# Performance work log

Measured on AMD Instinct MI355X. Metric: run time of the kernel, lower is better.

Reference implementation:

```python
import jax, jax.numpy as jnp
import numpy as np

EPS = 1e-6


def setup_inputs() -> dict:
    key = jax.random.key(0)
    ks = jax.random.split(key, 5)
    B, NH, S, DQK, DV = 2, 8, 1024, 256, 512
    return {
        "q": jax.random.normal(ks[0], (B, NH, S, DQK), dtype=jnp.float32),
        "k": jax.random.normal(ks[1], (B, NH, S, DQK), dtype=jnp.float32),
        "v": jax.random.normal(ks[2], (B, NH, S, DV), dtype=jnp.float32),
        "i_preact": jax.random.normal(ks[3], (B, NH, S), dtype=jnp.float32),
        "f_preact": jax.random.normal(ks[4], (B, NH, S), dtype=jnp.float32),
    }


def reference(q, k, v, i_preact, f_preact):
    B, NH, S, DQK = q.shape
    DV = v.shape[-1]
    inv_sqrt_d = jnp.asarray(1.0 / np.sqrt(DQK), dtype=q.dtype)
    eps = jnp.asarray(EPS, dtype=q.dtype)

    C0 = jnp.zeros((B, NH, DQK, DV), dtype=q.dtype)
    n0 = jnp.zeros((B, NH, DQK), dtype=q.dtype)
    m0 = jnp.zeros((B, NH), dtype=q.dtype)

    def step(carry, xs):
        C, n, m = carry
        q_t, k_t, v_t, i_t, f_t = xs  # [B,NH,DQK],[B,NH,DQK],[B,NH,DV],[B,NH],[B,NH]
        # f_log = -log(1 + exp(-f)) = log_sigmoid(f)
        f_log = jax.nn.log_sigmoid(f_t)
        m_new = jnp.maximum(f_log + m, i_t)
        f_gate = jnp.exp(f_log + m - m_new)
        i_gate = jnp.exp(i_t - m_new)
        kv_outer = k_t[..., :, None] * v_t[..., None, :]  # [B,NH,DQK,DV]
        C = f_gate[..., None, None] * C + i_gate[..., None, None] * kv_outer
        n = f_gate[..., None] * n + i_gate[..., None] * k_t
        q_scaled = q_t * inv_sqrt_d
        h_num = jnp.einsum("bhdv,bhd->bhv", C, q_scaled)
        qn_dot = jnp.sum(n * q_scaled, axis=-1, keepdims=True)  # [B,NH,1]
        h_den = jnp.maximum(jnp.abs(qn_dot), jnp.exp(-m_new)[..., None]) + eps
        h_t = h_num / h_den
        return (C, n, m_new), h_t

    # time-major scan over S
    xs = (
        jnp.moveaxis(q, 2, 0),
        jnp.moveaxis(k, 2, 0),
        jnp.moveaxis(v, 2, 0),
        jnp.moveaxis(i_preact, 2, 0),
        jnp.moveaxis(f_preact, 2, 0),
    )
    (C, n, m), h_tm = jax.lax.scan(step, (C0, n0, m0), xs)
    h = jnp.moveaxis(h_tm, 0, 2)  # [B,NH,S,DV]
    return h, C, n, m
```

## Files before the change

kernel.cpp:

```cpp
#include <hip/hip_runtime.h>
#include <math.h>

#define SEQ   1024
#define DQ    256
#define DVD   512
#define NHH   16
#define EPSF  1e-6f
#define INV_SQRT_D 0.0625f

typedef __attribute__((ext_vector_type(8)))  short short8v;
typedef __attribute__((ext_vector_type(16))) float f32x16;

#define WS_FG    0
#define WS_IG    (NHH*SEQ)
#define WS_ELIM  (2*NHH*SEQ)
#define WS_HDEN  (3*NHH*SEQ)
#define WS_AT    (4*NHH*SEQ)
#define WS_CS    (5*NHH*SEQ)
#define WS_UT    (6*NHH*SEQ)
#define WS_AC    (7*NHH*SEQ)
#define WS_BVEC  (WS_AC + NHH*16)
#define WS_SMALL_FLOATS (WS_BVEC + NHH*16*DQ)

#define QBF_OFF  ((size_t)WS_SMALL_FLOATS * 4)
#define KBF_OFF  (QBF_OFF + (size_t)NHH*SEQ*DQ*2)
#define VTB_OFF  (KBF_OFF + (size_t)NHH*SEQ*DQ*2)
#define KUT_OFF  (VTB_OFF + (size_t)NHH*DVD*SEQ*2)

__device__ __forceinline__ unsigned short f2bf(float f) {
  unsigned int u = __float_as_uint(f);
  return (unsigned short)((u + 0x7fffu + ((u >> 16) & 1u)) >> 16);
}

__device__ __forceinline__ void gl_lds16(const void* g, void* l) {
  __builtin_amdgcn_global_load_lds(
      (const __attribute__((address_space(1))) unsigned int*)g,
      (__attribute__((address_space(3))) unsigned int*)l, 16, 0, 0);
}

__global__ __launch_bounds__(1024) void gates_kernel(
    const float* __restrict__ ipre, const float* __restrict__ fpre,
    float* __restrict__ ws, float* __restrict__ m_out) {
  const int hh = blockIdx.x;
  const int t  = threadIdx.x;
  const int lane = t & 63, wid = t >> 6;
  __shared__ float Fs[SEQ];
  __shared__ float Ms[SEQ];
  __shared__ float wsum[16];
  __shared__ float wmax[16];

  const float fp = fpre[hh*SEQ + t];
  const float ip = ipre[hh*SEQ + t];
  const float flog = fminf(fp, 0.f) - log1pf(expf(-fabsf(fp)));

  float v = flog;
  #pragma unroll
  for (int off = 1; off < 64; off <<= 1) {
    float o = __shfl_up(v, off, 64);
    if (lane >= off) v += o;
  }
  if (lane == 63) wsum[wid] = v;
  __syncthreads();
  float woff = 0.f;
  #pragma unroll
  for (int i = 0; i < 16; ++i) { float s = wsum[i]; if (i < wid) woff += s; }
  const float F = v + woff;
  Fs[t] = F;

  float zm = ip - F;
  #pragma unroll
  for (int off = 1; off < 64; off <<= 1) {
    float o = __shfl_up(zm, off, 64);
    if (lane >= off) zm = fmaxf(zm, o);
  }
  if (lane == 63) wmax[wid] = zm;
  __syncthreads();
  float zoff = -INFINITY;
  #pragma unroll
  for (int i = 0; i < 16; ++i) { float s = wmax[i]; if (i < wid) zoff = fmaxf(zoff, s); }
  const float zfull = fmaxf(zm, zoff);
  const float m_t = F + fmaxf(zfull, 0.f);
  Ms[t] = m_t;
  __syncthreads();

  const float m_prev = (t == 0) ? 0.f : Ms[t - 1];
  const float F_end = Fs[SEQ-1], m_end = Ms[SEQ-1];

  ws[WS_FG   + hh*SEQ + t] = expf(flog + m_prev - m_t);
  ws[WS_IG   + hh*SEQ + t] = expf(ip - m_t);
  ws[WS_ELIM + hh*SEQ + t] = expf(-m_t);
  ws[WS_AT   + hh*SEQ + t] = F - m_t;
  ws[WS_CS   + hh*SEQ + t] = ip - F;
  ws[WS_UT   + hh*SEQ + t] = expf(F_end - F + ip - m_end);
  if (t == SEQ - 1) m_out[hh] = m_t;
  if ((t & 63) == 63) {
    const int c = t >> 6;
    const float Fprev  = (c == 0) ? 0.f : Fs[t - 64];
    const float mprevc = (c == 0) ? 0.f : Ms[t - 64];
    ws[WS_AC + hh*16 + c] = expf((F - Fprev) + (mprevc - m_t));
  }
}

__global__ __launch_bounds__(256) void prep_kernel(
    const float* __restrict__ kin, const float* __restrict__ vin,
    float* __restrict__ ws,
    unsigned short* __restrict__ k_bf, unsigned short* __restrict__ vt_bf,
    unsigned short* __restrict__ kut) {
  __shared__ float lk[64][257];
  const int b = blockIdx.x;
  if (b < 256) {
    const int hh = b >> 4, c = b & 15;
    const int d = threadIdx.x;
    const int tbase = hh*SEQ + c*64;
    const size_t base = (size_t)tbase * DQ;
    #pragma unroll 4
    for (int tt = 0; tt < 64; ++tt) {
      const float val = kin[base + (size_t)tt*DQ + d];
      lk[tt][d] = val;
      k_bf[base + (size_t)tt*DQ + d] = f2bf(val);
    }
    __syncthreads();
    const float* fg = ws + WS_FG + tbase;
    const float* ig = ws + WS_IG + tbase;
    float nb = 0.f;
    #pragma unroll 8
    for (int tt = 0; tt < 64; ++tt) nb = fg[tt]*nb + ig[tt]*lk[tt][d];
    ws[WS_BVEC + (hh*16 + c)*DQ + d] = nb;
    const float* u = ws + WS_UT + tbase;
    #pragma unroll
    for (int g = 0; g < 8; ++g) {
      short8v pk;
      #pragma unroll
      for (int j = 0; j < 8; ++j) {
        const int tt = g*8 + j;
        pk[j] = (short)f2bf(u[tt] * lk[tt][d]);
      }
      *(short8v*)(kut + ((size_t)(hh*DQ + d))*SEQ + c*64 + g*8) = pk;
    }
  } else {
    const int b2 = b - 256;
    const int hh = b2 >> 5, tg = b2 & 31;
    const int tx = threadIdx.x & 31, ty = threadIdx.x >> 5;
    float (*tile)[33] = (float(*)[33])lk;
    for (int vt = 0; vt < 16; ++vt) {
      #pragma unroll
      for (int i = 0; i < 4; ++i)
        tile[ty + 8*i][tx] =
            vin[((size_t)(hh*SEQ + tg*32 + ty + 8*i))*DVD + vt*32 + tx];
      __syncthreads();
      #pragma unroll
      for (int i = 0; i < 4; ++i)
        vt_bf[((size_t)(hh*DVD + vt*32 + ty + 8*i))*SEQ + tg*32 + tx] =
            f2bf(tile[tx][ty + 8*i]);
      __syncthreads();
    }
  }
}

__global__ __launch_bounds__(256) void hden_kernel(
    const float* __restrict__ kin, const float* __restrict__ qin,
    float* __restrict__ ws, unsigned short* __restrict__ q_bf,
    float* __restrict__ n_out) {
  const int hh = blockIdx.x >> 4;
  const int c  = blockIdx.x & 15;
  const int d  = threadIdx.x;
  __shared__ float pbuf[64][DQ];
  __shared__ float spart[64][4];

  float n = 0.f;
  for (int j = 0; j < c; ++j)
    n = ws[WS_AC + hh*16 + j]*n + ws[WS_BVEC + (hh*16 + j)*DQ + d];
  if (c == 15) {
    const float nf = ws[WS_AC + hh*16 + 15]*n +
                     ws[WS_BVEC + (hh*16 + 15)*DQ + d];
    n_out[hh*DQ + d] = nf;
  }

  const int tbase = hh*SEQ + c*64;
  const size_t base = (size_t)tbase * DQ;
  #pragma unroll 4
  for (int tt = 0; tt < 64; ++tt) {
    const float fg = ws[WS_FG + tbase + tt];
    const float ig = ws[WS_IG + tbase + tt];
    n = fg*n + ig*kin[base + (size_t)tt*DQ + d];
    const float qv = qin[base + (size_t)tt*DQ + d];
    q_bf[base + (size_t)tt*DQ + d] = f2bf(qv * INV_SQRT_D);
    pbuf[tt][d] = n * qv;
  }
  __syncthreads();

  {
    const int tt = d >> 2, qd = d & 3;
    float s = 0.f;
    #pragma unroll 8
    for (int j = 0; j < 64; ++j)
      s += pbuf[tt][qd*64 + ((j + d) & 63)];
    spart[tt][qd] = s;
  }
  __syncthreads();
  if (d < 64) {
    const float tot = (spart[d][0] + spart[d][1]) + (spart[d][2] + spart[d][3]);
    const float qn = tot * INV_SQRT_D;
    const float hd = fmaxf(fabsf(qn), ws[WS_ELIM + tbase + d]) + EPSF;
    ws[WS_HDEN + tbase + d] = hd;
  }
}

__global__ __launch_bounds__(512, 2) void attn_kernel(
    const unsigned short* __restrict__ q_bf,
    const unsigned short* __restrict__ k_bf,
    const unsigned short* __restrict__ vt_bf,
    const float* __restrict__ ws,
    float* __restrict__ h_out) {
  const int b = blockIdx.x;
  const int phase = b >> 8;
  const int idx = b & 255;
  const int hh = idx & 15;
  const int vh = (idx >> 4) & 1;
  const int qq = idx >> 5;
  const int qi = phase ? (15 - qq) : qq;
  const int nch = (qi >> 1) + 1;

  const int tid = threadIdx.x;
  const int w = tid >> 6, lane = tid & 63, l31 = lane & 31, hl = lane >> 5;
  const int tsub = w >> 2;
  const int sblk = w & 3;
  const int vsub = w & 3;

  __shared__ unsigned short Klds[128*256];
  __shared__ unsigned short Vtlds[256*128];
  __shared__ unsigned short Plds[64*128];
  __shared__ float c_lds[128];

  const float* a_g  = ws + WS_AT;
  const float* c_g  = ws + WS_CS;
  const float* hd_g = ws + WS_HDEN;

  const int tq = qi*64 + tsub*32 + l31;
  const float a_t = a_g[hh*SEQ + tq];

  short8v qfrag[16];
  #pragma unroll
  for (int d = 0; d < 16; ++d)
    qfrag[d] = *(const short8v*)(q_bf + ((size_t)(hh*SEQ + tq))*DQ + d*16 + hl*8);

  f32x16 acc0 = {}, acc1 = {};

  auto stage = [&](int c) {
    const int s0 = c*128;
    #pragma unroll
    for (int p = 0; p < 8; ++p) {
      int u = p*512 + tid;
      int row = u >> 5, slot = u & 31;
      const unsigned short* src = k_bf +
          ((size_t)(hh*SEQ + s0 + row))*DQ + ((slot ^ (row & 31))*8);
      gl_lds16(src, (char*)Klds + (p*8 + w)*1024);
    }
    #pragma unroll
    for (int p = 0; p < 8; ++p) {
      int u = p*512 + tid;
      int row = u >> 4, slot = u & 15;
      const unsigned short* src = vt_bf +
          ((size_t)(hh*DVD + vh*256 + row))*SEQ + s0 + ((slot ^ (row & 15))*8);
      gl_lds16(src, (char*)Vtlds + (p*8 + w)*1024);
    }
    if (tid < 128) c_lds[tid] = c_g[hh*SEQ + s0 + tid];
  };

  stage(0);
  __syncthreads();

  for (int c = 0; c < nch; ++c) {
    const int s0 = c*128;
    f32x16 sacc = {};
    const int srow = sblk*32 + l31;
    #pragma unroll
    for (int d = 0; d < 16; ++d) {
      short8v af = *(const short8v*)&Klds[srow*256 + (((d*2 + hl) ^ (srow & 31))*8)];
      sacc = __builtin_amdgcn_mfma_f32_32x32x16_bf16(af, qfrag[d], sacc, 0, 0, 0);
    }
    const int prow = tsub*32 + l31;
    #pragma unroll
    for (int i = 0; i < 8; ++i) {
      const int r0 = 2*i;
      const int sl = sblk*32 + (r0 & 3) + 8*(r0 >> 2) + 4*hl;
      const int sg = s0 + sl;
      const float c0 = c_lds[sl];
      const float c1 = c_lds[sl + 1];
      const float p0 = (sg     <= tq) ? __expf(a_t + c0) * sacc[r0]     : 0.f;
      const float p1 = (sg + 1 <= tq) ? __expf(a_t + c1) * sacc[r0 + 1] : 0.f;
      unsigned int pk;
      asm volatile("v_cvt_pk_bf16_f32 %0, %1, %2" : "=v"(pk) : "v"(p0), "v"(p1));
      const int byte = sl*2;
      const int slot = byte >> 4, rem = byte & 15;
      *(unsigned int*)((char*)Plds + prow*256 + ((slot ^ (prow & 15))<<4) + rem) = pk;
    }
    __syncthreads();

    #pragma unroll
    for (int ss = 0; ss < 8; ++ss) {
      const int arow = tsub*32 + l31;
      short8v pa = *(const short8v*)&Plds[arow*128 + (((ss*2 + hl) ^ (arow & 15))*8)];
      const int vr0 = vsub*64 + l31;
      const int slotB = (ss*2 + hl) ^ (l31 & 15);
      short8v vb0 = *(const short8v*)&Vtlds[vr0*128 + slotB*8];
      short8v vb1 = *(const short8v*)&Vtlds[(vr0 + 32)*128 + slotB*8];
      acc0 = __builtin_amdgcn_mfma_f32_32x32x16_bf16(pa, vb0, acc0, 0, 0, 0);
      acc1 = __builtin_amdgcn_mfma_f32_32x32x16_bf16(pa, vb1, acc1, 0, 0, 0);
    }
    __syncthreads();
    if (c + 1 < nch) { stage(c + 1); __syncthreads(); }
  }

  #pragma unroll
  for (int r = 0; r < 16; ++r) {
    const int tl = tsub*32 + (r & 3) + 8*(r >> 2) + 4*hl;
    const int tg = qi*64 + tl;
    const float inv = 1.0f / hd_g[hh*SEQ + tg];
    const size_t ob = ((size_t)(hh*SEQ + tg))*DVD + vh*256 + vsub*64 + l31;
    h_out[ob]      = acc0[r] * inv;
    h_out[ob + 32] = acc1[r] * inv;
  }
}

__global__ __launch_bounds__(256, 2) void cgemm_kernel(
    const unsigned short* __restrict__ kut,
    const unsigned short* __restrict__ vt,
    float* __restrict__ C_out) {
  const int b = blockIdx.x;
  const int hh = b >> 4;
  const int mt = (b >> 3) & 1;
  const int nt = b & 7;
  const int tid = threadIdx.x;
  const int w = tid >> 6, lane = tid & 63, l31 = lane & 31, hl = lane >> 5;
  const int mr = w >> 1;
  const int nc = w & 1;

  __shared__ unsigned short Alds[128*64];
  __shared__ unsigned short Blds[64*64];

  f32x16 acc0 = {}, acc1 = {};
  for (int c = 0; c < 16; ++c) {
    const int t0 = c*64;
    #pragma unroll
    for (int p = 0; p < 4; ++p) {
      int u = p*256 + tid; int row = u >> 3, slot = u & 7;
      const unsigned short* src = kut +
          ((size_t)(hh*DQ + mt*128 + row))*SEQ + t0 + ((slot ^ (row & 7))*8);
      gl_lds16(src, (char*)Alds + (p*4 + w)*1024);
    }
    #pragma unroll
    for (int p = 0; p < 2; ++p) {
      int u = p*256 + tid; int row = u >> 3, slot = u & 7;
      const unsigned short* src = vt +
          ((size_t)(hh*DVD + nt*64 + row))*SEQ + t0 + ((slot ^ (row & 7))*8);
      gl_lds16(src, (char*)Blds + (p*4 + w)*1024);
    }
    __syncthreads();
    #pragma unroll
    for (int ks = 0; ks < 4; ++ks) {
      const int br = nc*32 + l31;
      short8v bf_ = *(const short8v*)&Blds[br*64 + (((ks*2 + hl) ^ (br & 7))*8)];
      const int ar0 = mr*64 + l31, ar1 = ar0 + 32;
      short8v a0 = *(const short8v*)&Alds[ar0*64 + (((ks*2 + hl) ^ (ar0 & 7))*8)];
      short8v a1 = *(const short8v*)&Alds[ar1*64 + (((ks*2 + hl) ^ (ar1 & 7))*8)];
      acc0 = __builtin_amdgcn_mfma_f32_32x32x16_bf16(a0, bf_, acc0, 0, 0, 0);
      acc1 = __builtin_amdgcn_mfma_f32_32x32x16_bf16(a1, bf_, acc1, 0, 0, 0);
    }
    __syncthreads();
  }
  #pragma unroll
  for (int r = 0; r < 16; ++r) {
    const int dl = (r & 3) + 8*(r >> 2) + 4*hl;
    const int d0 = mt*128 + mr*64 + dl;
    const size_t ob = ((size_t)(hh*DQ + d0))*DVD + nt*64 + nc*32 + l31;
    C_out[ob]            = acc0[r];
    C_out[ob + 32*DVD]   = acc1[r];
  }
}

extern "C" void kernel_launch(void* const* d_in, const int* in_sizes, int n_in,
                              void* d_out, int out_size, void* d_ws, size_t ws_size,
                              hipStream_t stream) {
  const float* q  = (const float*)d_in[0];
  const float* k  = (const float*)d_in[1];
  const float* v  = (const float*)d_in[2];
  const float* ip = (const float*)d_in[3];
  const float* fp = (const float*)d_in[4];

  float* h_out = (float*)d_out;
  float* C_out = h_out + (size_t)NHH*SEQ*DVD;
  float* n_out = C_out + (size_t)NHH*DQ*DVD;
  float* m_out = n_out + NHH*DQ;
  float* ws    = (float*)d_ws;

  unsigned short* q_bf  = (unsigned short*)((char*)d_ws + QBF_OFF);
  unsigned short* k_bf  = (unsigned short*)((char*)d_ws + KBF_OFF);
  unsigned short* vt_bf = (unsigned short*)((char*)d_ws + VTB_OFF);
  unsigned short* kut   = (unsigned short*)((char*)d_ws + KUT_OFF);

  gates_kernel<<<NHH, 1024, 0, stream>>>(ip, fp, ws, m_out);
  prep_kernel<<<768, 256, 0, stream>>>(k, v, ws, k_bf, vt_bf, kut);
  hden_kernel<<<NHH*16, 256, 0, stream>>>(k, q, ws, q_bf, n_out);
  attn_kernel<<<512, 512, 0, stream>>>(q_bf, k_bf, vt_bf, ws, h_out);
  cgemm_kernel<<<256, 256, 0, stream>>>(kut, vt_bf, C_out);
}
```

Measured before the change: 100.7 us.

## Fuse gate scan into prep kernel and pair causal query tiles per block

The separate gates kernel is removed. Each k-prep block now recomputes the full per-head log-sigmoid prefix sum and running max over 1024 steps, and keeps its chunk's forget, input and u gates in shared memory instead of reading them from the workspace. Block 0 of each head still writes the shared gate arrays to the workspace. The attention kernel goes from 512 to 256 blocks, and each block handles a long and a short causal query tile (15-pr and pr) in sequence so the work per block is even. This saves one launch and a global round trip but adds redundant scan work per block, and it halves the number of attention blocks resident at once.

Result: no change. 99.73 us (-0.9%).

```diff
diff --git a/kernel.cpp b/kernel.cpp
--- a/kernel.cpp
+++ b/kernel.cpp
@@ -17,8 +17,7 @@
 #define WS_HDEN  (3*NHH*SEQ)
 #define WS_AT    (4*NHH*SEQ)
 #define WS_CS    (5*NHH*SEQ)
-#define WS_UT    (6*NHH*SEQ)
-#define WS_AC    (7*NHH*SEQ)
+#define WS_AC    (6*NHH*SEQ)
 #define WS_BVEC  (WS_AC + NHH*16)
 #define WS_SMALL_FLOATS (WS_BVEC + NHH*16*DQ)
 
@@ -38,102 +37,136 @@
       (__attribute__((address_space(3))) unsigned int*)l, 16, 0, 0);
 }
 
-__global__ __launch_bounds__(1024) void gates_kernel(
-    const float* __restrict__ ipre, const float* __restrict__ fpre,
-    float* __restrict__ ws, float* __restrict__ m_out) {
-  const int hh = blockIdx.x;
-  const int t  = threadIdx.x;
-  const int lane = t & 63, wid = t >> 6;
-  __shared__ float Fs[SEQ];
-  __shared__ float Ms[SEQ];
-  __shared__ float wsum[16];
-  __shared__ float wmax[16];
-
-  const float fp = fpre[hh*SEQ + t];
-  const float ip = ipre[hh*SEQ + t];
-  const float flog = fminf(fp, 0.f) - log1pf(expf(-fabsf(fp)));
-
-  float v = flog;
-  #pragma unroll
-  for (int off = 1; off < 64; off <<= 1) {
-    float o = __shfl_up(v, off, 64);
-    if (lane >= off) v += o;
-  }
-  if (lane == 63) wsum[wid] = v;
-  __syncthreads();
-  float woff = 0.f;
-  #pragma unroll
-  for (int i = 0; i < 16; ++i) { float s = wsum[i]; if (i < wid) woff += s; }
-  const float F = v + woff;
-  Fs[t] = F;
-
-  float zm = ip - F;
-  #pragma unroll
-  for (int off = 1; off < 64; off <<= 1) {
-    float o = __shfl_up(zm, off, 64);
-    if (lane >= off) zm = fmaxf(zm, o);
-  }
-  if (lane == 63) wmax[wid] = zm;
-  __syncthreads();
-  float zoff = -INFINITY;
-  #pragma unroll
-  for (int i = 0; i < 16; ++i) { float s = wmax[i]; if (i < wid) zoff = fmaxf(zoff, s); }
-  const float zfull = fmaxf(zm, zoff);
-  const float m_t = F + fmaxf(zfull, 0.f);
-  Ms[t] = m_t;
-  __syncthreads();
-
-  const float m_prev = (t == 0) ? 0.f : Ms[t - 1];
-  const float F_end = Fs[SEQ-1], m_end = Ms[SEQ-1];
-
-  ws[WS_FG   + hh*SEQ + t] = expf(flog + m_prev - m_t);
-  ws[WS_IG   + hh*SEQ + t] = expf(ip - m_t);
-  ws[WS_ELIM + hh*SEQ + t] = expf(-m_t);
-  ws[WS_AT   + hh*SEQ + t] = F - m_t;
-  ws[WS_CS   + hh*SEQ + t] = ip - F;
-  ws[WS_UT   + hh*SEQ + t] = expf(F_end - F + ip - m_end);
-  if (t == SEQ - 1) m_out[hh] = m_t;
-  if ((t & 63) == 63) {
-    const int c = t >> 6;
-    const float Fprev  = (c == 0) ? 0.f : Fs[t - 64];
-    const float mprevc = (c == 0) ? 0.f : Ms[t - 64];
-    ws[WS_AC + hh*16 + c] = expf((F - Fprev) + (mprevc - m_t));
-  }
-}
-
 __global__ __launch_bounds__(256) void prep_kernel(
     const float* __restrict__ kin, const float* __restrict__ vin,
+    const float* __restrict__ ipre, const float* __restrict__ fpre,
     float* __restrict__ ws,
     unsigned short* __restrict__ k_bf, unsigned short* __restrict__ vt_bf,
-    unsigned short* __restrict__ kut) {
+    unsigned short* __restrict__ kut, float* __restrict__ m_out) {
   __shared__ float lk[64][257];
+  __shared__ float swsum[4], swmax[4];
+  __shared__ float bndF[16], bndM[16], fin2[2];
+  __shared__ float cfg[64], cig[64], cut[64];
+
   const int b = blockIdx.x;
   if (b < 256) {
     const int hh = b >> 4, c = b & 15;
     const int d = threadIdx.x;
+    const int lane = d & 63, wid = d >> 6;
     const int tbase = hh*SEQ + c*64;
     const size_t base = (size_t)tbase * DQ;
+
     #pragma unroll 4
     for (int tt = 0; tt < 64; ++tt) {
       const float val = kin[base + (size_t)tt*DQ + d];
       lk[tt][d] = val;
       k_bf[base + (size_t)tt*DQ + d] = f2bf(val);
     }
-    __syncthreads();
-    const float* fg = ws + WS_FG + tbase;
-    const float* ig = ws + WS_IG + tbase;
+
+    const float4 f4 = *(const float4*)(fpre + hh*SEQ + 4*d);
+    const float4 i4 = *(const float4*)(ipre + hh*SEQ + 4*d);
+    float fv[4] = {f4.x, f4.y, f4.z, f4.w};
+    float iv[4] = {i4.x, i4.y, i4.z, i4.w};
+    float fl[4], F[4];
+    float s = 0.f;
+    #pragma unroll
+    for (int j = 0; j < 4; ++j) {
+      fl[j] = fminf(fv[j], 0.f) - log1pf(expf(-fabsf(fv[j])));
+      s += fl[j]; F[j] = s;
+    }
+    float wsc = s;
+    #pragma unroll
+    for (int off = 1; off < 64; off <<= 1) {
+      float o = __shfl_up(wsc, off, 64);
+      if (lane >= off) wsc += o;
+    }
+    if (lane == 63) swsum[wid] = wsc;
+    __syncthreads();
+    float woff = 0.f;
+    #pragma unroll
+    for (int i = 0; i < 4; ++i) { float t = swsum[i]; if (i < wid) woff += t; }
+    const float Fexc = woff + (wsc - s);
+    #pragma unroll
+    for (int j = 0; j < 4; ++j) F[j] += Fexc;
+
+    float zser[4];
+    float zs = -INFINITY;
+    #pragma unroll
+    for (int j = 0; j < 4; ++j) {
+      zs = fmaxf(zs, iv[j] - F[j]); zser[j] = zs;
+    }
+    float zmI = zs;
+    #pragma unroll
+    for (int off = 1; off < 64; off <<= 1) {
+      float o = __shfl_up(zmI, off, 64);
+      if (lane >= off) zmI = fmaxf(zmI, o);
+    }
+    if (lane == 63) swmax[wid] = zmI;
+    float zexcl = __shfl_up(zmI, 1, 64);
+    if (lane == 0) zexcl = -INFINITY;
+    __syncthreads();
+    float zoffW = -INFINITY;
+    #pragma unroll
+    for (int i = 0; i < 4; ++i) { float t = swmax[i]; if (i < wid) zoffW = fmaxf(zoffW, t); }
+    const float zPexc = fmaxf(zoffW, zexcl);
+
+    float mprev = Fexc + fmaxf(zPexc, 0.f);
+    float m_[4], fg_[4], ig_[4];
+    #pragma unroll
+    for (int j = 0; j < 4; ++j) {
+      const float zP = fmaxf(zPexc, zser[j]);
+      m_[j] = F[j] + fmaxf(zP, 0.f);
+      fg_[j] = expf(fl[j] + mprev - m_[j]);
+      ig_[j] = expf(iv[j] - m_[j]);
+      mprev = m_[j];
+    }
+
+    if ((d & 15) == 15) { bndF[d >> 4] = F[3]; bndM[d >> 4] = m_[3]; }
+    if (d == 255)       { fin2[0] = F[3]; fin2[1] = m_[3]; }
+    const int q0 = d - 16*c;
+    if (q0 >= 0 && q0 < 16) {
+      #pragma unroll
+      for (int j = 0; j < 4; ++j) { cfg[q0*4 + j] = fg_[j]; cig[q0*4 + j] = ig_[j]; }
+    }
+    if (c == 0) {
+      float4 o;
+      o.x=fg_[0]; o.y=fg_[1]; o.z=fg_[2]; o.w=fg_[3];
+      *(float4*)(ws + WS_FG + hh*SEQ + 4*d) = o;
+      o.x=ig_[0]; o.y=ig_[1]; o.z=ig_[2]; o.w=ig_[3];
+      *(float4*)(ws + WS_IG + hh*SEQ + 4*d) = o;
+      o.x=expf(-m_[0]); o.y=expf(-m_[1]); o.z=expf(-m_[2]); o.w=expf(-m_[3]);
+      *(float4*)(ws + WS_ELIM + hh*SEQ + 4*d) = o;
+      o.x=F[0]-m_[0]; o.y=F[1]-m_[1]; o.z=F[2]-m_[2]; o.w=F[3]-m_[3];
+      *(float4*)(ws + WS_AT + hh*SEQ + 4*d) = o;
+      o.x=iv[0]-F[0]; o.y=iv[1]-F[1]; o.z=iv[2]-F[2]; o.w=iv[3]-F[3];
+      *(float4*)(ws + WS_CS + hh*SEQ + 4*d) = o;
+      if (d == 255) m_out[hh] = m_[3];
+    }
+    __syncthreads();
+    if (c == 0 && d < 16) {
+      const float Fp = d ? bndF[d-1] : 0.f;
+      const float mp = d ? bndM[d-1] : 0.f;
+      ws[WS_AC + hh*16 + d] = expf((bndF[d] - Fp) + (mp - bndM[d]));
+    }
+    if (q0 >= 0 && q0 < 16) {
+      const float Fe = fin2[0], me = fin2[1];
+      #pragma unroll
+      for (int j = 0; j < 4; ++j)
+        cut[q0*4 + j] = expf(Fe - F[j] + iv[j] - me);
+    }
+    __syncthreads();
+
     float nb = 0.f;
     #pragma unroll 8
-    for (int tt = 0; tt < 64; ++tt) nb = fg[tt]*nb + ig[tt]*lk[tt][d];
+    for (int tt = 0; tt < 64; ++tt) nb = cfg[tt]*nb + cig[tt]*lk[tt][d];
     ws[WS_BVEC + (hh*16 + c)*DQ + d] = nb;
-    const float* u = ws + WS_UT + tbase;
     #pragma unroll
     for (int g = 0; g < 8; ++g) {
       short8v pk;
       #pragma unroll
       for (int j = 0; j < 8; ++j) {
         const int tt = g*8 + j;
-        pk[j] = (short)f2bf(u[tt] * lk[tt][d]);
+        pk[j] = (short)f2bf(cut[tt] * lk[tt][d]);
       }
       *(short8v*)(kut + ((size_t)(hh*DQ + d))*SEQ + c*64 + g*8) = pk;
     }
@@ -212,14 +245,10 @@
     const unsigned short* __restrict__ vt_bf,
     const float* __restrict__ ws,
     float* __restrict__ h_out) {
-  const int b = blockIdx.x;
-  const int phase = b >> 8;
-  const int idx = b & 255;
+  const int idx = blockIdx.x;
   const int hh = idx & 15;
-  const int vh = (idx >> 4) & 1;
-  const int qq = idx >> 5;
-  const int qi = phase ? (15 - qq) : qq;
-  const int nch = (qi >> 1) + 1;
+  const int pr = (idx >> 4) & 7;
+  const int vh = idx >> 7;
 
   const int tid = threadIdx.x;
   const int w = tid >> 6, lane = tid & 63, l31 = lane & 31, hl = lane >> 5;
@@ -235,16 +264,6 @@
   const float* a_g  = ws + WS_AT;
   const float* c_g  = ws + WS_CS;
   const float* hd_g = ws + WS_HDEN;
-
-  const int tq = qi*64 + tsub*32 + l31;
-  const float a_t = a_g[hh*SEQ + tq];
-
-  short8v qfrag[16];
-  #pragma unroll
-  for (int d = 0; d < 16; ++d)
-    qfrag[d] = *(const short8v*)(q_bf + ((size_t)(hh*SEQ + tq))*DQ + d*16 + hl*8);
-
-  f32x16 acc0 = {}, acc1 = {};
 
   auto stage = [&](int c) {
     const int s0 = c*128;
@@ -267,59 +286,73 @@
     if (tid < 128) c_lds[tid] = c_g[hh*SEQ + s0 + tid];
   };
 
-  stage(0);
-  __syncthreads();
-
-  for (int c = 0; c < nch; ++c) {
-    const int s0 = c*128;
-    f32x16 sacc = {};
-    const int srow = sblk*32 + l31;
-    #pragma unroll
-    for (int d = 0; d < 16; ++d) {
-      short8v af = *(const short8v*)&Klds[srow*256 + (((d*2 + hl) ^ (srow & 31))*8)];
-      sacc = __builtin_amdgcn_mfma_f32_32x32x16_bf16(af, qfrag[d], sacc, 0, 0, 0);
-    }
-    const int prow = tsub*32 + l31;
-    #pragma unroll
-    for (int i = 0; i < 8; ++i) {
-      const int r0 = 2*i;
-      const int sl = sblk*32 + (r0 & 3) + 8*(r0 >> 2) + 4*hl;
-      const int sg = s0 + sl;
-      const float c0 = c_lds[sl];
-      const float c1 = c_lds[sl + 1];
-      const float p0 = (sg     <= tq) ? __expf(a_t + c0) * sacc[r0]     : 0.f;
-      const float p1 = (sg + 1 <= tq) ? __expf(a_t + c1) * sacc[r0 + 1] : 0.f;
-      unsigned int pk;
-      asm volatile("v_cvt_pk_bf16_f32 %0, %1, %2" : "=v"(pk) : "v"(p0), "v"(p1));
-      const int byte = sl*2;
-      const int slot = byte >> 4, rem = byte & 15;
-      *(unsigned int*)((char*)Plds + prow*256 + ((slot ^ (prow & 15))<<4) + rem) = pk;
-    }
-    __syncthreads();
-
-    #pragma unroll
-    for (int ss = 0; ss < 8; ++ss) {
-      const int arow = tsub*32 + l31;
-      short8v pa = *(const short8v*)&Plds[arow*128 + (((ss*2 + hl) ^ (arow & 15))*8)];
-      const int vr0 = vsub*64 + l31;
-      const int slotB = (ss*2 + hl) ^ (l31 & 15);
-      short8v vb0 = *(const short8v*)&Vtlds[vr0*128 + slotB*8];
-      short8v vb1 = *(const short8v*)&Vtlds[(vr0 + 32)*128 + slotB*8];
-      acc0 = __builtin_amdgcn_mfma_f32_32x32x16_bf16(pa, vb0, acc0, 0, 0, 0);
-      acc1 = __builtin_amdgcn_mfma_f32_32x32x16_bf16(pa, vb1, acc1, 0, 0, 0);
-    }
-    __syncthreads();
-    if (c + 1 < nch) { stage(c + 1); __syncthreads(); }
-  }
-
-  #pragma unroll
-  for (int r = 0; r < 16; ++r) {
-    const int tl = tsub*32 + (r & 3) + 8*(r >> 2) + 4*hl;
-    const int tg = qi*64 + tl;
-    const float inv = 1.0f / hd_g[hh*SEQ + tg];
-    const size_t ob = ((size_t)(hh*SEQ + tg))*DVD + vh*256 + vsub*64 + l31;
-    h_out[ob]      = acc0[r] * inv;
-    h_out[ob + 32] = acc1[r] * inv;
+  for (int tile = 0; tile < 2; ++tile) {
+    const int qi  = tile ? pr : (15 - pr);
+    const int nch = (qi >> 1) + 1;
+
+    const int tq = qi*64 + tsub*32 + l31;
+    const float a_t = a_g[hh*SEQ + tq];
+    short8v qfrag[16];
+    #pragma unroll
+    for (int d = 0; d < 16; ++d)
+      qfrag[d] = *(const short8v*)(q_bf + ((size_t)(hh*SEQ + tq))*DQ + d*16 + hl*8);
+
+    f32x16 acc0 = {}, acc1 = {};
+
+    stage(0);
+    __syncthreads();
+
+    for (int c = 0; c < nch; ++c) {
+      const int s0 = c*128;
+      f32x16 sacc = {};
+      const int srow = sblk*32 + l31;
+      #pragma unroll
+      for (int d = 0; d < 16; ++d) {
+        short8v af = *(const short8v*)&Klds[srow*256 + (((d*2 + hl) ^ (srow & 31))*8)];
+        sacc = __builtin_amdgcn_mfma_f32_32x32x16_bf16(af, qfrag[d], sacc, 0, 0, 0);
+      }
+      const int prow = tsub*32 + l31;
+      #pragma unroll
+      for (int i = 0; i < 8; ++i) {
+        const int r0 = 2*i;
+        const int sl = sblk*32 + (r0 & 3) + 8*(r0 >> 2) + 4*hl;
+        const int sg = s0 + sl;
+        const float c0 = c_lds[sl];
+        const float c1 = c_lds[sl + 1];
+        const float p0 = (sg     <= tq) ? __expf(a_t + c0) * sacc[r0]     : 0.f;
+        const float p1 = (sg + 1 <= tq) ? __expf(a_t + c1) * sacc[r0 + 1] : 0.f;
+        unsigned int pk;
+        asm volatile("v_cvt_pk_bf16_f32 %0, %1, %2" : "=v"(pk) : "v"(p0), "v"(p1));
+        const int byte = sl*2;
+        const int slot = byte >> 4, rem = byte & 15;
+        *(unsigned int*)((char*)Plds + prow*256 + ((slot ^ (prow & 15))<<4) + rem) = pk;
+      }
+      __syncthreads();
+
+      #pragma unroll
+      for (int ss = 0; ss < 8; ++ss) {
+        const int arow = tsub*32 + l31;
+        short8v pa = *(const short8v*)&Plds[arow*128 + (((ss*2 + hl) ^ (arow & 15))*8)];
+        const int vr0 = vsub*64 + l31;
+        const int slotB = (ss*2 + hl) ^ (l31 & 15);
+        short8v vb0 = *(const short8v*)&Vtlds[vr0*128 + slotB*8];
+        short8v vb1 = *(const short8v*)&Vtlds[(vr0 + 32)*128 + slotB*8];
+        acc0 = __builtin_amdgcn_mfma_f32_32x32x16_bf16(pa, vb0, acc0, 0, 0, 0);
+        acc1 = __builtin_amdgcn_mfma_f32_32x32x16_bf16(pa, vb1, acc1, 0, 0, 0);
+      }
+      __syncthreads();
+      if (c + 1 < nch) { stage(c + 1); __syncthreads(); }
+    }
+
+    #pragma unroll
+    for (int r = 0; r < 16; ++r) {
+      const int tl = tsub*32 + (r & 3) + 8*(r >> 2) + 4*hl;
+      const int tg = qi*64 + tl;
+      const float inv = 1.0f / hd_g[hh*SEQ + tg];
+      const size_t ob = ((size_t)(hh*SEQ + tg))*DVD + vh*256 + vsub*64 + l31;
+      h_out[ob]      = acc0[r] * inv;
+      h_out[ob + 32] = acc1[r] * inv;
+    }
   }
 }
 
@@ -399,9 +432,8 @@
   unsigned short* vt_bf = (unsigned short*)((char*)d_ws + VTB_OFF);
   unsigned short* kut   = (unsigned short*)((char*)d_ws + KUT_OFF);
 
-  gates_kernel<<<NHH, 1024, 0, stream>>>(ip, fp, ws, m_out);
-  prep_kernel<<<768, 256, 0, stream>>>(k, v, ws, k_bf, vt_bf, kut);
+  prep_kernel<<<768, 256, 0, stream>>>(k, v, ip, fp, ws, k_bf, vt_bf, kut, m_out);
   hden_kernel<<<NHH*16, 256, 0, stream>>>(k, q, ws, q_bf, n_out);
-  attn_kernel<<<512, 512, 0, stream>>>(q_bf, k_bf, vt_bf, ws, h_out);
+  attn_kernel<<<256, 512, 0, stream>>>(q_bf, k_bf, vt_bf, ws, h_out);
   cgemm_kernel<<<256, 256, 0, stream>>>(kut, vt_bf, C_out);
 }
```
